# Kernel tuning notes

Measured on AMD Instinct MI355X. Metric: run time of the kernel, lower is better.

Reference implementation:

```python
import jax, jax.numpy as jnp
import numpy as np

B, GX, GY = 4, 480, 360
C_IN, C_OUT = 64, 32
N = 480000

def setup_inputs() -> dict:
    key = jax.random.key(0)
    k1, k2, k3, k4, k5 = jax.random.split(key, 5)
    pt_fea = jax.random.normal(k1, (N, C_IN), dtype=jnp.float32)
    pt_ind = jax.random.randint(k2, (N, 2), 0, 360, dtype=jnp.int32)
    batch_idx = jax.random.randint(k3, (N,), 0, B, dtype=jnp.int32)
    W_comp = jax.random.normal(k4, (C_IN, C_OUT), dtype=jnp.float32) * 0.1
    b_comp = jax.random.normal(k5, (C_OUT,), dtype=jnp.float32) * 0.1
    return {"pt_fea": pt_fea, "pt_ind": pt_ind, "batch_idx": batch_idx,
            "W_comp": W_comp, "b_comp": b_comp}

def reference(pt_fea, pt_ind, batch_idx, W_comp, b_comp):
    # Linearized voxel key: (batch, x, y) -> flat segment id.
    # torch.unique + scatter_max over unique voxels followed by fancy-index
    # scatter into a zero grid is equivalent to a dense segment_max with
    # empty voxels forced to zero.
    seg = (batch_idx.astype(jnp.int32) * (GX * GY)
           + pt_ind[:, 0] * GY + pt_ind[:, 1])  # [N]
    num_seg = B * GX * GY
    pooled = jax.ops.segment_max(pt_fea, seg, num_segments=num_seg)  # [BV, C_IN]
    cnt = jax.ops.segment_sum(jnp.ones((pt_fea.shape[0],), jnp.float32), seg,
                              num_segments=num_seg)  # [BV]
    occupied = (cnt > 0)[:, None]
    pooled = jnp.where(occupied, pooled, 0.0)  # neutralize -inf of empty voxels
    # fea_compression: Linear + ReLU, applied to occupied voxels only
    comp = jax.nn.relu(pooled @ W_comp + b_comp)  # [BV, C_OUT]
    comp = jnp.where(occupied, comp, 0.0)
    out = comp.reshape(B, GX, GY, C_OUT)
    return jnp.transpose(out, (0, 3, 1, 2))  # [B, C_OUT, GX, GY]
```

## Files before the change

kernel.cpp:

```cpp
#include <hip/hip_runtime.h>

#define GXGY  172800
#define NSEG  691200
#define CIN   64
#define COUT  32
#define VPB   64
#define PSTR  (CIN + 1)

__global__ __launch_bounds__(256) void build_lists_kernel(
    const int* __restrict__ ind,
    const int* __restrict__ bidx,
    int*       __restrict__ head,
    int*       __restrict__ next,
    int N)
{
    int i = blockIdx.x * 256 + threadIdx.x;
    if (i >= N) return;
    int2 xy = ((const int2*)ind)[i];
    int seg = bidx[i] * GXGY + xy.x * 360 + xy.y;
    next[i] = atomicExch(&head[seg], i);
}

__global__ __launch_bounds__(256) void pool_compress_kernel(
    const float* __restrict__ fea,
    const int*   __restrict__ head,
    const int*   __restrict__ next,
    const float* __restrict__ W,
    const float* __restrict__ bias,
    float*       __restrict__ out)
{
    __shared__ float sW[CIN * COUT];
    __shared__ float sb[COUT];
    __shared__ float sP[VPB * PSTR];
    __shared__ int   sOcc[VPB];

    int tid  = threadIdx.x;
    int wid  = tid >> 6;
    int lane = tid & 63;

    for (int j = tid; j < CIN * COUT; j += 256) sW[j] = W[j];
    if (tid < COUT) sb[tid] = bias[tid];

    int vbase = blockIdx.x * VPB;

    int myhead = (lane < 16) ? head[vbase + wid * 16 + lane] : -1;

    for (int j = 0; j < 16; ++j) {
        int lv = wid * 16 + j;
        int i = __shfl(myhead, j);
        if (i < 0) {
            if (lane == 0) sOcc[lv] = 0;
            continue;
        }
        if (lane == 0) sOcc[lv] = 1;
        float m = fea[(size_t)i * CIN + lane];
        i = next[i];
        while (i >= 0) {
            m = fmaxf(m, fea[(size_t)i * CIN + lane]);
            i = next[i];
        }
        sP[lv * PSTR + lane] = m;
    }
    __syncthreads();

    int lv = lane;
    int g  = wid;
    int v  = vbase + lv;
    int b  = v / GXGY;
    int rem = v - b * GXGY;

    float res[8];
    if (sOcc[lv]) {
        float acc[8];
        #pragma unroll
        for (int c = 0; c < 8; ++c) acc[c] = sb[g * 8 + c];
        #pragma unroll
        for (int k = 0; k < CIN; ++k) {
            float p = sP[lv * PSTR + k];
            const float* w = &sW[k * COUT + g * 8];
            #pragma unroll
            for (int c = 0; c < 8; ++c) acc[c] = fmaf(p, w[c], acc[c]);
        }
        #pragma unroll
        for (int c = 0; c < 8; ++c) res[c] = fmaxf(acc[c], 0.0f);
    } else {
        #pragma unroll
        for (int c = 0; c < 8; ++c) res[c] = 0.0f;
    }

    float* op = out + (size_t)b * COUT * GXGY + (size_t)g * 8 * GXGY + rem;
    #pragma unroll
    for (int c = 0; c < 8; ++c) op[c * GXGY] = res[c];
}

extern "C" void kernel_launch(void* const* d_in, const int* in_sizes, int n_in,
                              void* d_out, int out_size, void* d_ws, size_t ws_size,
                              hipStream_t stream)
{
    const float* fea  = (const float*)d_in[0];
    const int*   ind  = (const int*)d_in[1];
    const int*   bidx = (const int*)d_in[2];
    const float* W    = (const float*)d_in[3];
    const float* bias = (const float*)d_in[4];
    float*       out  = (float*)d_out;

    int N = in_sizes[0] / CIN;

    int* head = (int*)d_ws;
    int* next = (int*)d_ws + NSEG;

    hipMemsetAsync(head, 0xFF, (size_t)NSEG * sizeof(int), stream);
    build_lists_kernel<<<(N + 255) / 256, 256, 0, stream>>>(ind, bidx, head, next, N);
    pool_compress_kernel<<<NSEG / VPB, 256, 0, stream>>>(fea, head, next, W, bias, out);
}
```

Measured before the change: 306.3 us.

## Vectorize gather with float4 quarter-wave lists and read weights via scalar loads

The pooling gather now splits each wave into four 16-lane groups, each walking one voxel's linked list and loading features as float4, so four lists are traversed concurrently per wave instead of one. The per-block shared-memory copy of W and bias is removed; weights are read directly from global memory with a wave-uniform group index so they can use scalar loads. Batch index computation is hoisted to the block level. The intent is more memory-level parallelism on the pointer-chasing gather and less staging overhead per block, at the cost of more divergence within a wave when list lengths differ.

```diff
diff --git a/kernel.cpp b/kernel.cpp
--- a/kernel.cpp
+++ b/kernel.cpp
@@ -5,7 +5,7 @@
 #define CIN   64
 #define COUT  32
 #define VPB   64
-#define PSTR  (CIN + 1)
+#define PSTR  65
 
 __global__ __launch_bounds__(256) void build_lists_kernel(
     const int* __restrict__ ind,
@@ -29,57 +29,60 @@
     const float* __restrict__ bias,
     float*       __restrict__ out)
 {
-    __shared__ float sW[CIN * COUT];
-    __shared__ float sb[COUT];
     __shared__ float sP[VPB * PSTR];
     __shared__ int   sOcc[VPB];
 
     int tid  = threadIdx.x;
     int wid  = tid >> 6;
     int lane = tid & 63;
-
-    for (int j = tid; j < CIN * COUT; j += 256) sW[j] = W[j];
-    if (tid < COUT) sb[tid] = bias[tid];
+    int sub  = lane >> 4;
+    int sl   = lane & 15;
 
     int vbase = blockIdx.x * VPB;
 
-    int myhead = (lane < 16) ? head[vbase + wid * 16 + lane] : -1;
+    int heads = (lane < 16) ? head[vbase + wid * 16 + lane] : -1;
 
-    for (int j = 0; j < 16; ++j) {
-        int lv = wid * 16 + j;
-        int i = __shfl(myhead, j);
-        if (i < 0) {
-            if (lane == 0) sOcc[lv] = 0;
-            continue;
+    for (int j = 0; j < 4; ++j) {
+        int lv = wid * 16 + j * 4 + sub;
+        int i = __shfl(heads, j * 4 + sub);
+        if (sl == 0) sOcc[lv] = (i >= 0) ? 1 : 0;
+        if (i >= 0) {
+            const float4* fp = (const float4*)(fea + (size_t)i * CIN) + sl;
+            float4 m = *fp;
+            i = next[i];
+            while (i >= 0) {
+                float4 t = *((const float4*)(fea + (size_t)i * CIN) + sl);
+                m.x = fmaxf(m.x, t.x);
+                m.y = fmaxf(m.y, t.y);
+                m.z = fmaxf(m.z, t.z);
+                m.w = fmaxf(m.w, t.w);
+                i = next[i];
+            }
+            float* dst = &sP[lv * PSTR + sl * 4];
+            dst[0] = m.x; dst[1] = m.y; dst[2] = m.z; dst[3] = m.w;
         }
-        if (lane == 0) sOcc[lv] = 1;
-        float m = fea[(size_t)i * CIN + lane];
-        i = next[i];
-        while (i >= 0) {
-            m = fmaxf(m, fea[(size_t)i * CIN + lane]);
-            i = next[i];
-        }
-        sP[lv * PSTR + lane] = m;
     }
     __syncthreads();
 
     int lv = lane;
-    int g  = wid;
-    int v  = vbase + lv;
-    int b  = v / GXGY;
-    int rem = v - b * GXGY;
+    int g  = __builtin_amdgcn_readfirstlane(wid);
+    int b  = vbase / GXGY;
+    int rem = vbase - b * GXGY + lv;
+
+    const float* Wg = W + g * 8;
+    const float* bg = bias + g * 8;
 
     float res[8];
     if (sOcc[lv]) {
         float acc[8];
         #pragma unroll
-        for (int c = 0; c < 8; ++c) acc[c] = sb[g * 8 + c];
-        #pragma unroll
+        for (int c = 0; c < 8; ++c) acc[c] = bg[c];
+        #pragma unroll 16
         for (int k = 0; k < CIN; ++k) {
             float p = sP[lv * PSTR + k];
-            const float* w = &sW[k * COUT + g * 8];
             #pragma unroll
-            for (int c = 0; c < 8; ++c) acc[c] = fmaf(p, w[c], acc[c]);
+            for (int c = 0; c < 8; ++c)
+                acc[c] = fmaf(p, Wg[k * COUT + c], acc[c]);
         }
         #pragma unroll
         for (int c = 0; c < 8; ++c) res[c] = fmaxf(acc[c], 0.0f);
```

After: 258.7 us. 15.5% less time.
